# Optimization experiments

Measured on AMD Instinct MI355X. Metric: run time of the kernel, lower is better.

Reference implementation:

```python
import jax, jax.numpy as jnp
import numpy as np

GAMMA = 0.99          # discount factor from __init__
TD_LAMBDA = 0.95      # lambda for GAE (lambda < 1 -> GAE branch)
STEP_TYPE_LAST = 2    # alf StepType.LAST


def setup_inputs() -> dict:
    key = jax.random.key(0)
    k0, k1, k2, k3, k4 = jax.random.split(key, 5)
    T1, B = 1024, 4096  # [T+1, B] time-major
    return {
        "value": jax.random.normal(k0, (T1, B), jnp.float32),
        "target_value": jax.random.normal(k1, (T1, B), jnp.float32),
        "reward": jax.random.normal(k2, (T1, B), jnp.float32),
        "step_type": jax.random.randint(k3, (T1, B), 0, 3, jnp.int32),
        "discount": jax.random.uniform(k4, (T1, B), dtype=jnp.float32),
    }


def _gae(reward, target_value, step_type, discount):
    # discounts passed to value_ops are training_info.discount * gamma
    d = discount * GAMMA                                   # [T+1, B]
    is_last = (step_type == STEP_TYPE_LAST).astype(reward.dtype)
    # one-step TD residuals, time-major [T, B]
    delta = reward[1:] + d[1:] * target_value[1:] - target_value[:-1]
    wd = d[1:] * TD_LAMBDA                                 # [T, B]
    not_last = 1.0 - is_last[:-1]                          # [T, B]

    def step(adv_next, xs):
        delta_t, wd_t, nl_t = xs
        adv = nl_t * (delta_t + wd_t * adv_next)
        return adv, adv

    init = jnp.zeros_like(reward[0])                       # [B]
    _, advs = jax.lax.scan(step, init, (delta, wd, not_last), reverse=True)
    return advs                                            # [T, B]


def reference(value, target_value, reward, step_type, discount):
    advs = jax.lax.stop_gradient(_gae(reward, target_value, step_type, discount))
    returns = advs + target_value[:-1]                     # G_t^lambda, [T, B]
    # element_wise_squared_loss(returns.detach(), value[:-1])
    td_err = jax.lax.stop_gradient(returns) - value[:-1]
    loss = td_err * td_err                                 # [T, B]
    # tensor_extend_zero: append a zero row -> [T+1, B]
    return jnp.concatenate([loss, jnp.zeros_like(loss[:1])], axis=0)
```

## Files before the change

### kernel.cpp

```cpp
#include <hip/hip_runtime.h>

#define T1     1024
#define T      1023
#define B      4096
#define LOGB   12
#define CHUNK  16
#define NCHUNK 64

#define GAMMA     0.99f
#define TD_LAMBDA 0.95f

__global__ __launch_bounds__(256) void k_compose(
    const float* __restrict__ tv, const float* __restrict__ rew,
    const int* __restrict__ st, const float* __restrict__ disc,
    float* __restrict__ Ac, float* __restrict__ Bc)
{
    int tid = blockIdx.x * blockDim.x + threadIdx.x;
    int b = tid & (B - 1);
    int c = tid >> LOGB;
    int s = c * CHUNK;
    int e = min(s + CHUNK, T);

    float A = 0.f, Bf = 1.f;
    float tv_next = tv[(size_t)e * B + b];
    for (int t = e - 1; t >= s; --t) {
        size_t idx  = (size_t)t * B + b;
        size_t idx1 = idx + B;
        float d1    = disc[idx1] * GAMMA;
        float tv_t  = tv[idx];
        float delta = rew[idx1] + d1 * tv_next - tv_t;
        float wd    = d1 * TD_LAMBDA;
        float nl    = (st[idx] == 2) ? 0.f : 1.f;
        float a  = nl * delta;
        float bb = nl * wd;
        A  = fmaf(bb, A, a);
        Bf = bb * Bf;
        tv_next = tv_t;
    }
    Ac[tid] = A;
    Bc[tid] = Bf;
}

__global__ __launch_bounds__(256) void k_scan(
    const float* __restrict__ Ac, const float* __restrict__ Bc,
    float* __restrict__ R)
{
    int b = blockIdx.x * blockDim.x + threadIdx.x;
    float adv = 0.f;
    for (int c = NCHUNK - 1; c >= 0; --c) {
        int i = c * B + b;
        R[i] = adv;
        adv = fmaf(Bc[i], adv, Ac[i]);
    }
}

__global__ __launch_bounds__(256) void k_replay(
    const float* __restrict__ value, const float* __restrict__ tv,
    const float* __restrict__ rew, const int* __restrict__ st,
    const float* __restrict__ disc, const float* __restrict__ R,
    float* __restrict__ out)
{
    int tid = blockIdx.x * blockDim.x + threadIdx.x;
    int b = tid & (B - 1);
    int c = tid >> LOGB;
    int s = c * CHUNK;
    int e = min(s + CHUNK, T);

    float adv = R[tid];
    float tv_next = tv[(size_t)e * B + b];
    if (c == NCHUNK - 1) {
        out[(size_t)T * B + b] = 0.f;
    }
    for (int t = e - 1; t >= s; --t) {
        size_t idx  = (size_t)t * B + b;
        size_t idx1 = idx + B;
        float d1    = disc[idx1] * GAMMA;
        float tv_t  = tv[idx];
        float delta = rew[idx1] + d1 * tv_next - tv_t;
        float wd    = d1 * TD_LAMBDA;
        float nl    = (st[idx] == 2) ? 0.f : 1.f;
        adv = nl * fmaf(wd, adv, delta);
        float td = adv + tv_t - value[idx];
        out[idx] = td * td;
        tv_next = tv_t;
    }
}

extern "C" void kernel_launch(void* const* d_in, const int* in_sizes, int n_in,
                              void* d_out, int out_size, void* d_ws, size_t ws_size,
                              hipStream_t stream) {
    const float* value = (const float*)d_in[0];
    const float* tv    = (const float*)d_in[1];
    const float* rew   = (const float*)d_in[2];
    const int*   st    = (const int*)d_in[3];
    const float* disc  = (const float*)d_in[4];
    float* out = (float*)d_out;

    float* Ac = (float*)d_ws;
    float* Bc = Ac + (size_t)NCHUNK * B;
    float* R  = Bc + (size_t)NCHUNK * B;

    k_compose<<<(NCHUNK * B) / 256, 256, 0, stream>>>(tv, rew, st, disc, Ac, Bc);
    k_scan<<<B / 256, 256, 0, stream>>>(Ac, Bc, R);
    k_replay<<<(NCHUNK * B) / 256, 256, 0, stream>>>(value, tv, rew, st, disc, R, out);
}
```

Baseline: 133.3 us.

## Fuse compose/scan/replay into single-pass GAE kernel with decoupled lookback

Replaces the three-kernel chunked scan with a single kernel. Each block composes its time chunk, keeps the per-step coefficients in registers, publishes its aggregate through a flag, waits for all later chunks' flags and then folds their aggregates directly. This removes the second read of the inputs and the separate serial scan kernel. In exchange it depends on inter-block spin-waiting. Blocks are ordered so later-time chunks launch first, so forward progress relies on block scheduling order, and each block redundantly folds up to 63 aggregates.

New measurement: 265.0 us. +98.8%, slower.

```diff
diff --git a/kernel.cpp b/kernel.cpp
--- a/kernel.cpp
+++ b/kernel.cpp
@@ -1,88 +1,99 @@
 #include <hip/hip_runtime.h>
 
-#define T1     1024
 #define T      1023
 #define B      4096
-#define LOGB   12
 #define CHUNK  16
 #define NCHUNK 64
+#define NCB    16
+#define NBLK   (NCHUNK * NCB)
 
 #define GAMMA     0.99f
 #define TD_LAMBDA 0.95f
 
-__global__ __launch_bounds__(256) void k_compose(
-    const float* __restrict__ tv, const float* __restrict__ rew,
-    const int* __restrict__ st, const float* __restrict__ disc,
-    float* __restrict__ Ac, float* __restrict__ Bc)
+__global__ void k_zero(int* __restrict__ flags) { flags[threadIdx.x] = 0; }
+
+__global__ __launch_bounds__(256, 4) void k_gae(
+    const float* __restrict__ value, const float* __restrict__ tv,
+    const float* __restrict__ rew, const int* __restrict__ st,
+    const float* __restrict__ disc,
+    float* __restrict__ AggA, float* __restrict__ AggB,
+    int* __restrict__ flags, float* __restrict__ out)
 {
-    int tid = blockIdx.x * blockDim.x + threadIdx.x;
-    int b = tid & (B - 1);
-    int c = tid >> LOGB;
-    int s = c * CHUNK;
-    int e = min(s + CHUNK, T);
+    const int bid = blockIdx.x;
+    const int cb  = bid & (NCB - 1);
+    const int c   = (NCHUNK - 1) - (bid >> 4);
+    const int col = cb * 256 + threadIdx.x;
+    const int s   = c * CHUNK;
+
+    float a[CHUNK], b[CHUNK], m[CHUNK];
 
     float A = 0.f, Bf = 1.f;
-    float tv_next = tv[(size_t)e * B + b];
-    for (int t = e - 1; t >= s; --t) {
-        size_t idx  = (size_t)t * B + b;
-        size_t idx1 = idx + B;
-        float d1    = disc[idx1] * GAMMA;
-        float tv_t  = tv[idx];
-        float delta = rew[idx1] + d1 * tv_next - tv_t;
-        float wd    = d1 * TD_LAMBDA;
-        float nl    = (st[idx] == 2) ? 0.f : 1.f;
-        float a  = nl * delta;
-        float bb = nl * wd;
-        A  = fmaf(bb, A, a);
-        Bf = bb * Bf;
-        tv_next = tv_t;
+    float tvn = tv[min(s + CHUNK, T) * B + col];
+    #pragma unroll
+    for (int k = CHUNK - 1; k >= 0; --k) {
+        const int t = s + k;
+        if (t < T) {
+            const int i0 = t * B + col;
+            const int i1 = i0 + B;
+            const float d1    = disc[i1] * GAMMA;
+            const float tvt   = tv[i0];
+            const float delta = rew[i1] + d1 * tvn - tvt;
+            const float nl    = (st[i0] == 2) ? 0.f : 1.f;
+            a[k] = nl * delta;
+            b[k] = nl * (d1 * TD_LAMBDA);
+            m[k] = tvt - value[i0];
+            A  = fmaf(b[k], A, a[k]);
+            Bf *= b[k];
+            tvn = tvt;
+        } else { a[k] = 0.f; b[k] = 1.f; m[k] = 0.f; }
     }
-    Ac[tid] = A;
-    Bc[tid] = Bf;
-}
 
-__global__ __launch_bounds__(256) void k_scan(
-    const float* __restrict__ Ac, const float* __restrict__ Bc,
-    float* __restrict__ R)
-{
-    int b = blockIdx.x * blockDim.x + threadIdx.x;
+    const int ag = c * B + col;
+    AggA[ag] = A;
+    AggB[ag] = Bf;
+    __threadfence();
+    __syncthreads();
+    if (threadIdx.x == 0)
+        __hip_atomic_store(&flags[c * NCB + cb], 1,
+                           __ATOMIC_RELEASE, __HIP_MEMORY_SCOPE_AGENT);
+
+    const int num = (NCHUNK - 1) - c;
+    for (int i = threadIdx.x; i < num; i += 256) {
+        const int f = (c + 1 + i) * NCB + cb;
+        while (__hip_atomic_load(&flags[f], __ATOMIC_RELAXED,
+                                 __HIP_MEMORY_SCOPE_AGENT) == 0) {}
+    }
+    __syncthreads();
+    __builtin_amdgcn_fence(__ATOMIC_ACQUIRE, "agent");
+
     float adv = 0.f;
-    for (int c = NCHUNK - 1; c >= 0; --c) {
-        int i = c * B + b;
-        R[i] = adv;
-        adv = fmaf(Bc[i], adv, Ac[i]);
+    int cc = NCHUNK - 1;
+    while (cc > c) {
+        float Ab[8], Bb[8];
+        #pragma unroll
+        for (int k = 0; k < 8; ++k) {
+            const int ccc = cc - k;
+            const int i = (ccc > c ? ccc : cc) * B + col;
+            Ab[k] = AggA[i];
+            Bb[k] = AggB[i];
+            if (ccc <= c) { Ab[k] = 0.f; Bb[k] = 1.f; }
+        }
+        #pragma unroll
+        for (int k = 0; k < 8; ++k)
+            adv = fmaf(Bb[k], adv, Ab[k]);
+        cc -= 8;
     }
-}
 
-__global__ __launch_bounds__(256) void k_replay(
-    const float* __restrict__ value, const float* __restrict__ tv,
-    const float* __restrict__ rew, const int* __restrict__ st,
-    const float* __restrict__ disc, const float* __restrict__ R,
-    float* __restrict__ out)
-{
-    int tid = blockIdx.x * blockDim.x + threadIdx.x;
-    int b = tid & (B - 1);
-    int c = tid >> LOGB;
-    int s = c * CHUNK;
-    int e = min(s + CHUNK, T);
-
-    float adv = R[tid];
-    float tv_next = tv[(size_t)e * B + b];
-    if (c == NCHUNK - 1) {
-        out[(size_t)T * B + b] = 0.f;
-    }
-    for (int t = e - 1; t >= s; --t) {
-        size_t idx  = (size_t)t * B + b;
-        size_t idx1 = idx + B;
-        float d1    = disc[idx1] * GAMMA;
-        float tv_t  = tv[idx];
-        float delta = rew[idx1] + d1 * tv_next - tv_t;
-        float wd    = d1 * TD_LAMBDA;
-        float nl    = (st[idx] == 2) ? 0.f : 1.f;
-        adv = nl * fmaf(wd, adv, delta);
-        float td = adv + tv_t - value[idx];
-        out[idx] = td * td;
-        tv_next = tv_t;
+    if (c == NCHUNK - 1)
+        out[T * B + col] = 0.f;
+    #pragma unroll
+    for (int k = CHUNK - 1; k >= 0; --k) {
+        adv = fmaf(b[k], adv, a[k]);
+        const int t = s + k;
+        if (t < T) {
+            const float td = adv + m[k];
+            out[t * B + col] = td * td;
+        }
     }
 }
 
@@ -96,11 +107,11 @@
     const float* disc  = (const float*)d_in[4];
     float* out = (float*)d_out;
 
-    float* Ac = (float*)d_ws;
-    float* Bc = Ac + (size_t)NCHUNK * B;
-    float* R  = Bc + (size_t)NCHUNK * B;
+    float* AggA = (float*)d_ws;
+    float* AggB = AggA + (size_t)NCHUNK * B;
+    int*   flags = (int*)(AggB + (size_t)NCHUNK * B);
 
-    k_compose<<<(NCHUNK * B) / 256, 256, 0, stream>>>(tv, rew, st, disc, Ac, Bc);
-    k_scan<<<B / 256, 256, 0, stream>>>(Ac, Bc, R);
-    k_replay<<<(NCHUNK * B) / 256, 256, 0, stream>>>(value, tv, rew, st, disc, R, out);
+    k_zero<<<1, NBLK, 0, stream>>>(flags);
+    k_gae<<<NBLK, 256, 0, stream>>>(value, tv, rew, st, disc,
+                                    AggA, AggB, flags, out);
 }
```
